# Optimization experiments

Hardware: AMD Instinct MI355X
Metric: run time of the kernel (lower is better)

Reference implementation:

```python
import jax, jax.numpy as jnp
import numpy as np

B, H, S, D = 2, 16, 2048, 64

def setup_inputs() -> dict:
    key = jax.random.key(0)
    kq, kk, kv, km, ks = jax.random.split(key, 5)
    return {
        "query_input": jax.random.normal(kq, (B, H, S, D), dtype=jnp.float32),
        "key_input": jax.random.normal(kk, (B, H, S, D), dtype=jnp.float32),
        "value_input": jax.random.normal(kv, (B, H, S, D), dtype=jnp.float32),
        "query_mask": jnp.ones((B, 1, S, 1), dtype=jnp.float32),
        "key_mask": jax.random.uniform(km, (B, 1, 1, S), dtype=jnp.float32),
        "scale_factor": jax.random.normal(ks, (B, 1, 1, 1), dtype=jnp.float32),
        "dropout": 0,
    }

def reference(query_input, key_input, value_input, query_mask, key_mask, scale_factor, dropout):
    # qk = q @ k^T  -> [B, H, S, S]
    qk = jnp.einsum("bhqd,bhkd->bhqk", query_input, key_input)
    scaled_qk = qk * scale_factor                      # elementwise per-batch scale
    softmax_qk = jax.nn.softmax(scaled_qk, axis=-1)
    masked = softmax_qk * key_mask                     # post-softmax multiplicative mask
    # dropout with p=0 is the identity (deterministic baseline)
    output = jnp.einsum("bhqk,bhkd->bhqd", masked, value_input)
    return output
```

## Files before the change

### kernel.cpp

```cpp
#include <hip/hip_runtime.h>
#include <hip/hip_bf16.h>
#include <stdint.h>

#define BB 2
#define HH 16
#define SS 2048
#define DD 64
constexpr int BH = BB * HH;
constexpr int NT = SS / 64;
constexpr int QB = 16;

typedef _Float16 f16_t;
typedef f16_t f16x8 __attribute__((ext_vector_type(8)));
typedef float f32x4 __attribute__((ext_vector_type(4)));

__device__ __forceinline__ uint32_t pkf16(float a, float b) {
    return __builtin_bit_cast(uint32_t, __builtin_amdgcn_cvt_pkrtz(a, b));
}

__global__ __launch_bounds__(256)
void prepack(const float* __restrict__ Kg, const float* __restrict__ Vg,
             const float* __restrict__ Mg, f16_t* __restrict__ Kp,
             f16_t* __restrict__ Vp)
{
    __shared__ float Vs[64][65];
    const int bh = blockIdx.x % BH;
    const int kt = blockIdx.x / BH;
    const int b  = bh / HH;
    const int t  = threadIdx.x;
    const size_t gbase = (size_t)bh * SS * DD + (size_t)kt * 64 * DD;
    const size_t tbase = ((size_t)bh * NT + kt) * 4096;

    for (int c = t; c < 512; c += 256) {
        const int row = c >> 3, j = c & 7;
        const float* kp = Kg + gbase + (size_t)row * DD + j * 8;
        float4 a = *(const float4*)kp;
        float4 d = *(const float4*)(kp + 4);
        uint4 w = make_uint4(pkf16(a.x, a.y), pkf16(a.z, a.w),
                             pkf16(d.x, d.y), pkf16(d.z, d.w));
        *(uint4*)&Kp[tbase + (size_t)row * 64 + ((j ^ (row & 7)) * 8)] = w;
    }

    for (int c = t; c < 1024; c += 256) {
        const int key = c >> 4, dc = (c & 15) * 4;
        float4 v = *(const float4*)(Vg + gbase + (size_t)key * DD + dc);
        const float m = Mg[(size_t)b * SS + kt * 64 + key];
        Vs[key][dc + 0] = v.x * m;
        Vs[key][dc + 1] = v.y * m;
        Vs[key][dc + 2] = v.z * m;
        Vs[key][dc + 3] = v.w * m;
    }
    __syncthreads();

    for (int c = t; c < 512; c += 256) {
        const int dr = c >> 3, j = c & 7;
        float v0 = Vs[j * 8 + 0][dr], v1 = Vs[j * 8 + 1][dr];
        float v2 = Vs[j * 8 + 2][dr], v3 = Vs[j * 8 + 3][dr];
        float v4 = Vs[j * 8 + 4][dr], v5 = Vs[j * 8 + 5][dr];
        float v6 = Vs[j * 8 + 6][dr], v7 = Vs[j * 8 + 7][dr];
        uint4 w = make_uint4(pkf16(v0, v1), pkf16(v2, v3),
                             pkf16(v4, v5), pkf16(v6, v7));
        *(uint4*)&Vp[tbase + (size_t)dr * 64 + ((j ^ (dr & 7)) * 8)] = w;
    }
}

__global__ __launch_bounds__(512)
void fattn7(const float* __restrict__ Qg, const f16_t* __restrict__ Kp,
            const f16_t* __restrict__ Vp, const float* __restrict__ Sg,
            float* __restrict__ Og)
{
    __shared__ __align__(16) f16_t Kt[2][4096];
    __shared__ __align__(16) f16_t Vt[2][4096];
    __shared__ __align__(16) f16_t Pt[8][16][72];

    const int bh   = blockIdx.x % BH;
    const int qt   = blockIdx.x / BH;
    const int b    = bh / HH;
    const int tid  = threadIdx.x;
    const int wave = tid >> 6;
    const int lane = tid & 63;
    const int l16  = lane & 15;
    const int quad = lane >> 4;

    const float sc = Sg[b] * 1.44269504088896340736f;
    const size_t base = (size_t)bh * SS * DD;
    const size_t tb0  = (size_t)bh * NT * 4096;
    const int q0 = qt * 128 + wave * 16;

    auto stage = [&](int kt, int buf) {
        const f16_t* ks = Kp + tb0 + (size_t)kt * 4096 + tid * 8;
        const f16_t* vs = Vp + tb0 + (size_t)kt * 4096 + tid * 8;
        __builtin_amdgcn_global_load_lds(
            (const __attribute__((address_space(1))) void*)ks,
            (__attribute__((address_space(3))) void*)&Kt[buf][wave * 512],
            16, 0, 0);
        __builtin_amdgcn_global_load_lds(
            (const __attribute__((address_space(1))) void*)vs,
            (__attribute__((address_space(3))) void*)&Vt[buf][wave * 512],
            16, 0, 0);
    };

    stage(0, 0);

    f16x8 qf[2];
    {
        const float* qp = Qg + base + (size_t)(q0 + l16) * DD + quad * 8;
#pragma unroll
        for (int kc = 0; kc < 2; ++kc) {
            float4 a  = *(const float4*)(qp + kc * 32);
            float4 b4 = *(const float4*)(qp + kc * 32 + 4);
            f16x8 f;
            f[0] = (f16_t)(a.x * sc);  f[1] = (f16_t)(a.y * sc);
            f[2] = (f16_t)(a.z * sc);  f[3] = (f16_t)(a.w * sc);
            f[4] = (f16_t)(b4.x * sc); f[5] = (f16_t)(b4.y * sc);
            f[6] = (f16_t)(b4.z * sc); f[7] = (f16_t)(b4.w * sc);
            qf[kc] = f;
        }
    }

    f32x4 Ot[4];
#pragma unroll
    for (int mt = 0; mt < 4; ++mt) Ot[mt] = f32x4{0.f, 0.f, 0.f, 0.f};
    float m_run = -1e30f, l_run = 0.0f;

    const int swz = (l16 & 7) << 3;

    for (int kt = 0; kt < NT; ++kt) {
        const int cur = kt & 1;
        if (kt + 1 < NT) {
            stage(kt + 1, cur ^ 1);
            asm volatile("s_waitcnt vmcnt(2)" ::: "memory");
        } else {
            asm volatile("s_waitcnt vmcnt(0)" ::: "memory");
        }
        __builtin_amdgcn_s_barrier();

        f32x4 Sfr[4];
#pragma unroll
        for (int mt = 0; mt < 4; ++mt) {
            f32x4 acc = f32x4{0.f, 0.f, 0.f, 0.f};
#pragma unroll
            for (int kc = 0; kc < 2; ++kc) {
                const int off = (mt * 16 + l16) * 64 + ((kc * 32 + quad * 8) ^ swz);
                f16x8 kh = *(const f16x8*)&Kt[cur][off];
                acc = __builtin_amdgcn_mfma_f32_16x16x32_f16(kh, qf[kc], acc, 0, 0, 0);
            }
            Sfr[mt] = acc;
        }

        float m0 = fmaxf(fmaxf(Sfr[0][0], Sfr[0][1]), fmaxf(Sfr[0][2], Sfr[0][3]));
        float m1 = fmaxf(fmaxf(Sfr[1][0], Sfr[1][1]), fmaxf(Sfr[1][2], Sfr[1][3]));
        float m2 = fmaxf(fmaxf(Sfr[2][0], Sfr[2][1]), fmaxf(Sfr[2][2], Sfr[2][3]));
        float m3 = fmaxf(fmaxf(Sfr[3][0], Sfr[3][1]), fmaxf(Sfr[3][2], Sfr[3][3]));
        float mx = fmaxf(fmaxf(m0, m1), fmaxf(m2, m3));
        mx = fmaxf(mx, __shfl_xor(mx, 16));
        mx = fmaxf(mx, __shfl_xor(mx, 32));

        if (__any(mx > m_run)) {
            const float mnew  = fmaxf(m_run, mx);
            const float alpha = exp2f(m_run - mnew);
            m_run = mnew;
            l_run *= alpha;
#pragma unroll
            for (int mt = 0; mt < 4; ++mt) Ot[mt] *= alpha;
        }

        float ps[4][4];
        float rs = 0.0f;
#pragma unroll
        for (int mt = 0; mt < 4; ++mt)
#pragma unroll
            for (int r = 0; r < 4; ++r) {
                ps[mt][r] = exp2f(Sfr[mt][r] - m_run);
                rs += ps[mt][r];
            }
        rs += __shfl_xor(rs, 16);
        rs += __shfl_xor(rs, 32);
        l_run += rs;

#pragma unroll
        for (int mt = 0; mt < 4; ++mt) {
            uint2 w = make_uint2(pkf16(ps[mt][0], ps[mt][1]),
                                 pkf16(ps[mt][2], ps[mt][3]));
            *(uint2*)&Pt[wave][l16][mt * 16 + quad * 4] = w;
        }

#pragma unroll
        for (int kc = 0; kc < 2; ++kc) {
            f16x8 pf = *(const f16x8*)&Pt[wave][l16][kc * 32 + quad * 8];
#pragma unroll
            for (int mt = 0; mt < 4; ++mt) {
                const int off = (mt * 16 + l16) * 64 + ((kc * 32 + quad * 8) ^ swz);
                f16x8 vf = *(const f16x8*)&Vt[cur][off];
                Ot[mt] = __builtin_amdgcn_mfma_f32_16x16x32_f16(vf, pf, Ot[mt], 0, 0, 0);
            }
        }
        __builtin_amdgcn_s_barrier();
    }

    const float inv = 1.0f / l_run;
    float* op = Og + base + (size_t)(q0 + l16) * DD + quad * 4;
#pragma unroll
    for (int mt = 0; mt < 4; ++mt) {
#pragma unroll
        for (int r = 0; r < 4; ++r)
            op[mt * 16 + r] = Ot[mt][r] * inv;
    }
}

__global__ __launch_bounds__(512)
void fattn6(const float* __restrict__ Qg, const float* __restrict__ Kg,
            const float* __restrict__ Vg, const float* __restrict__ Mg,
            const float* __restrict__ Sg, float* __restrict__ Og)
{
    __shared__ __align__(16) f16_t Kh_lds[64][72];
    __shared__ __align__(16) f16_t Vt_lds[64][72];
    __shared__ __align__(16) f16_t Pt_lds[8][16][72];
    __shared__ float msk_lds[SS];

    const int bh   = blockIdx.x % BH;
    const int qt   = blockIdx.x / BH;
    const int b    = bh / HH;
    const int tid  = threadIdx.x;
    const int wave = tid >> 6;
    const int lane = tid & 63;
    const int l16  = lane & 15;
    const int quad = lane >> 4;

    const float sc = Sg[b] * 1.44269504088896340736f;
    const size_t base = (size_t)bh * SS * DD;
    const int q0 = qt * 128 + wave * 16;

    for (int i = tid; i < SS; i += 512) msk_lds[i] = Mg[(size_t)b * SS + i];

    f16x8 qf[2];
    {
        const float* qp = Qg + base + (size_t)(q0 + l16) * DD + quad * 8;
#pragma unroll
        for (int kc = 0; kc < 2; ++kc) {
            float4 a  = *(const float4*)(qp + kc * 32);
            float4 b4 = *(const float4*)(qp + kc * 32 + 4);
            f16x8 f;
            f[0] = (f16_t)(a.x * sc);  f[1] = (f16_t)(a.y * sc);
            f[2] = (f16_t)(a.z * sc);  f[3] = (f16_t)(a.w * sc);
            f[4] = (f16_t)(b4.x * sc); f[5] = (f16_t)(b4.y * sc);
            f[6] = (f16_t)(b4.z * sc); f[7] = (f16_t)(b4.w * sc);
            qf[kc] = f;
        }
    }

    f32x4 Ot[4];
#pragma unroll
    for (int mt = 0; mt < 4; ++mt) Ot[mt] = f32x4{0.f, 0.f, 0.f, 0.f};
    float m_run = -1e30f, l_run = 0.0f;

    const int krow = tid >> 3;
    const int kc8  = (tid & 7) * 8;
    const int vd   = tid & 63;
    const int vk0  = (tid >> 6) * 8;

    for (int kt = 0; kt < NT; ++kt) {
        __syncthreads();
        {
            const float* kp = Kg + base + (size_t)(kt * 64 + krow) * DD + kc8;
            float4 a0 = *(const float4*)(kp);
            float4 a1 = *(const float4*)(kp + 4);
            uint4 w = make_uint4(pkf16(a0.x, a0.y), pkf16(a0.z, a0.w),
                                 pkf16(a1.x, a1.y), pkf16(a1.z, a1.w));
            *(uint4*)&Kh_lds[krow][kc8] = w;
        }
        {
            const float* vp = Vg + base + (size_t)(kt * 64 + vk0) * DD + vd;
            const float* mp = &msk_lds[kt * 64 + vk0];
            float v0 = vp[0 * DD] * mp[0], v1 = vp[1 * DD] * mp[1];
            float v2 = vp[2 * DD] * mp[2], v3 = vp[3 * DD] * mp[3];
            float v4 = vp[4 * DD] * mp[4], v5 = vp[5 * DD] * mp[5];
            float v6 = vp[6 * DD] * mp[6], v7 = vp[7 * DD] * mp[7];
            uint4 w = make_uint4(pkf16(v0, v1), pkf16(v2, v3),
                                 pkf16(v4, v5), pkf16(v6, v7));
            *(uint4*)&Vt_lds[vd][vk0] = w;
        }
        __syncthreads();

        f32x4 Sfr[4];
#pragma unroll
        for (int mt = 0; mt < 4; ++mt) {
            f32x4 acc = f32x4{0.f, 0.f, 0.f, 0.f};
#pragma unroll
            for (int kc = 0; kc < 2; ++kc) {
                f16x8 kh = *(const f16x8*)&Kh_lds[mt * 16 + l16][kc * 32 + quad * 8];
                acc = __builtin_amdgcn_mfma_f32_16x16x32_f16(kh, qf[kc], acc, 0, 0, 0);
            }
            Sfr[mt] = acc;
        }

        float mx = Sfr[0][0];
#pragma unroll
        for (int mt = 0; mt < 4; ++mt)
#pragma unroll
            for (int r = 0; r < 4; ++r) mx = fmaxf(mx, Sfr[mt][r]);
        mx = fmaxf(mx, __shfl_xor(mx, 16));
        mx = fmaxf(mx, __shfl_xor(mx, 32));

        if (__any(mx > m_run)) {
            const float mnew  = fmaxf(m_run, mx);
            const float alpha = exp2f(m_run - mnew);
            m_run = mnew;
            l_run *= alpha;
#pragma unroll
            for (int mt = 0; mt < 4; ++mt) Ot[mt] *= alpha;
        }

        float ps[4][4];
        float rs = 0.0f;
#pragma unroll
        for (int mt = 0; mt < 4; ++mt)
#pragma unroll
            for (int r = 0; r < 4; ++r) {
                ps[mt][r] = exp2f(Sfr[mt][r] - m_run);
                rs += ps[mt][r];
            }
        rs += __shfl_xor(rs, 16);
        rs += __shfl_xor(rs, 32);
        l_run += rs;

#pragma unroll
        for (int mt = 0; mt < 4; ++mt) {
            uint2 w = make_uint2(pkf16(ps[mt][0], ps[mt][1]),
                                 pkf16(ps[mt][2], ps[mt][3]));
            *(uint2*)&Pt_lds[wave][l16][mt * 16 + quad * 4] = w;
        }

#pragma unroll
        for (int kc = 0; kc < 2; ++kc) {
            f16x8 pf = *(const f16x8*)&Pt_lds[wave][l16][kc * 32 + quad * 8];
#pragma unroll
            for (int mt = 0; mt < 4; ++mt) {
                f16x8 vf = *(const f16x8*)&Vt_lds[mt * 16 + l16][kc * 32 + quad * 8];
                Ot[mt] = __builtin_amdgcn_mfma_f32_16x16x32_f16(vf, pf, Ot[mt], 0, 0, 0);
            }
        }
    }

    const float inv = 1.0f / l_run;
    float* op = Og + base + (size_t)(q0 + l16) * DD + quad * 4;
#pragma unroll
    for (int mt = 0; mt < 4; ++mt) {
#pragma unroll
        for (int r = 0; r < 4; ++r)
            op[mt * 16 + r] = Ot[mt][r] * inv;
    }
}

extern "C" void kernel_launch(void* const* d_in, const int* in_sizes, int n_in,
                              void* d_out, int out_size, void* d_ws, size_t ws_size,
                              hipStream_t stream) {
    const float* Qg = (const float*)d_in[0];
    const float* Kg = (const float*)d_in[1];
    const float* Vg = (const float*)d_in[2];
    const float* Mg = (const float*)d_in[4];
    const float* Sg = (const float*)d_in[5];
    float* Og = (float*)d_out;

    const size_t kv_elems = (size_t)BH * SS * DD;
    const size_t need = 2 * kv_elems * sizeof(f16_t);

    if (d_ws != nullptr && ws_size >= need) {
        f16_t* Kp = (f16_t*)d_ws;
        f16_t* Vp = Kp + kv_elems;
        prepack<<<dim3(BH * NT), dim3(256), 0, stream>>>(Kg, Vg, Mg, Kp, Vp);
        fattn7<<<dim3(BH * QB), dim3(512), 0, stream>>>(Qg, Kp, Vp, Sg, Og);
    } else {
        fattn6<<<dim3(BH * QB), dim3(512), 0, stream>>>(Qg, Kg, Vg, Mg, Sg, Og);
    }
}
```

Measured before the change: 170.7 us.

## Software-pipeline PV matmul one tile behind QK with triple-buffered V

Restructures the flash-attention loop so the P·V MFMAs for the previous key tile run right after the current tile's QK MFMAs. This lets matrix work overlap the softmax ALU work, with V triple-buffered in LDS and one barrier per iteration instead of two. It also raises wave priority around the MFMA block, skips rescaling unless the running max grows by more than 8 (lazy rescale), and uses the raw hardware exp2 with tree-shaped reductions. The lazy rescale relies on fp16 P values tolerating up to 2^8 growth, and LDS use rises.

```diff
diff --git a/kernel.cpp b/kernel.cpp
--- a/kernel.cpp
+++ b/kernel.cpp
@@ -65,12 +65,12 @@
 }
 
 __global__ __launch_bounds__(512)
-void fattn7(const float* __restrict__ Qg, const f16_t* __restrict__ Kp,
+void fattn8(const float* __restrict__ Qg, const f16_t* __restrict__ Kp,
             const f16_t* __restrict__ Vp, const float* __restrict__ Sg,
             float* __restrict__ Og)
 {
     __shared__ __align__(16) f16_t Kt[2][4096];
-    __shared__ __align__(16) f16_t Vt[2][4096];
+    __shared__ __align__(16) f16_t Vt[3][4096];
     __shared__ __align__(16) f16_t Pt[8][16][72];
 
     const int bh   = blockIdx.x % BH;
@@ -87,20 +87,20 @@
     const size_t tb0  = (size_t)bh * NT * 4096;
     const int q0 = qt * 128 + wave * 16;
 
-    auto stage = [&](int kt, int buf) {
+    auto stage = [&](int kt, int kbuf, int vbuf) {
         const f16_t* ks = Kp + tb0 + (size_t)kt * 4096 + tid * 8;
         const f16_t* vs = Vp + tb0 + (size_t)kt * 4096 + tid * 8;
         __builtin_amdgcn_global_load_lds(
             (const __attribute__((address_space(1))) void*)ks,
-            (__attribute__((address_space(3))) void*)&Kt[buf][wave * 512],
+            (__attribute__((address_space(3))) void*)&Kt[kbuf][wave * 512],
             16, 0, 0);
         __builtin_amdgcn_global_load_lds(
             (const __attribute__((address_space(1))) void*)vs,
-            (__attribute__((address_space(3))) void*)&Vt[buf][wave * 512],
+            (__attribute__((address_space(3))) void*)&Vt[vbuf][wave * 512],
             16, 0, 0);
     };
 
-    stage(0, 0);
+    stage(0, 0, 0);
 
     f16x8 qf[2];
     {
@@ -125,16 +125,19 @@
 
     const int swz = (l16 & 7) << 3;
 
+    int vcur = 0;
     for (int kt = 0; kt < NT; ++kt) {
-        const int cur = kt & 1;
+        const int kcur = kt & 1;
+        const int vnxt = (vcur == 2) ? 0 : vcur + 1;
         if (kt + 1 < NT) {
-            stage(kt + 1, cur ^ 1);
+            stage(kt + 1, kcur ^ 1, vnxt);
             asm volatile("s_waitcnt vmcnt(2)" ::: "memory");
         } else {
             asm volatile("s_waitcnt vmcnt(0)" ::: "memory");
         }
         __builtin_amdgcn_s_barrier();
 
+        __builtin_amdgcn_s_setprio(1);
         f32x4 Sfr[4];
 #pragma unroll
         for (int mt = 0; mt < 4; ++mt) {
@@ -142,23 +145,41 @@
 #pragma unroll
             for (int kc = 0; kc < 2; ++kc) {
                 const int off = (mt * 16 + l16) * 64 + ((kc * 32 + quad * 8) ^ swz);
-                f16x8 kh = *(const f16x8*)&Kt[cur][off];
+                f16x8 kh = *(const f16x8*)&Kt[kcur][off];
                 acc = __builtin_amdgcn_mfma_f32_16x16x32_f16(kh, qf[kc], acc, 0, 0, 0);
             }
             Sfr[mt] = acc;
         }
 
-        float m0 = fmaxf(fmaxf(Sfr[0][0], Sfr[0][1]), fmaxf(Sfr[0][2], Sfr[0][3]));
-        float m1 = fmaxf(fmaxf(Sfr[1][0], Sfr[1][1]), fmaxf(Sfr[1][2], Sfr[1][3]));
-        float m2 = fmaxf(fmaxf(Sfr[2][0], Sfr[2][1]), fmaxf(Sfr[2][2], Sfr[2][3]));
-        float m3 = fmaxf(fmaxf(Sfr[3][0], Sfr[3][1]), fmaxf(Sfr[3][2], Sfr[3][3]));
-        float mx = fmaxf(fmaxf(m0, m1), fmaxf(m2, m3));
+        if (kt > 0) {
+            const int vprv = (vcur == 0) ? 2 : vcur - 1;
+#pragma unroll
+            for (int kc = 0; kc < 2; ++kc) {
+                f16x8 pf = *(const f16x8*)&Pt[wave][l16][kc * 32 + quad * 8];
+#pragma unroll
+                for (int mt = 0; mt < 4; ++mt) {
+                    const int off = (mt * 16 + l16) * 64 + ((kc * 32 + quad * 8) ^ swz);
+                    f16x8 vf = *(const f16x8*)&Vt[vprv][off];
+                    Ot[mt] = __builtin_amdgcn_mfma_f32_16x16x32_f16(vf, pf, Ot[mt], 0, 0, 0);
+                }
+            }
+        }
+        __builtin_amdgcn_s_setprio(0);
+
+        float a0 = fmaxf(fmaxf(Sfr[0][0], Sfr[0][1]), Sfr[0][2]);
+        float b0 = fmaxf(fmaxf(Sfr[1][0], Sfr[1][1]), Sfr[1][2]);
+        a0 = fmaxf(fmaxf(a0, Sfr[0][3]), Sfr[2][0]);
+        b0 = fmaxf(fmaxf(b0, Sfr[1][3]), Sfr[2][1]);
+        a0 = fmaxf(fmaxf(a0, Sfr[2][2]), Sfr[3][0]);
+        b0 = fmaxf(fmaxf(b0, Sfr[2][3]), Sfr[3][1]);
+        a0 = fmaxf(fmaxf(a0, Sfr[3][2]), Sfr[3][3]);
+        float mx = fmaxf(a0, b0);
         mx = fmaxf(mx, __shfl_xor(mx, 16));
         mx = fmaxf(mx, __shfl_xor(mx, 32));
 
-        if (__any(mx > m_run)) {
+        if (__any(mx > m_run + 8.0f)) {
             const float mnew  = fmaxf(m_run, mx);
-            const float alpha = exp2f(m_run - mnew);
+            const float alpha = __builtin_amdgcn_exp2f(m_run - mnew);
             m_run = mnew;
             l_run *= alpha;
 #pragma unroll
@@ -166,14 +187,17 @@
         }
 
         float ps[4][4];
-        float rs = 0.0f;
 #pragma unroll
         for (int mt = 0; mt < 4; ++mt)
 #pragma unroll
-            for (int r = 0; r < 4; ++r) {
-                ps[mt][r] = exp2f(Sfr[mt][r] - m_run);
-                rs += ps[mt][r];
-            }
+            for (int r = 0; r < 4; ++r)
+                ps[mt][r] = __builtin_amdgcn_exp2f(Sfr[mt][r] - m_run);
+
+        float s0 = (ps[0][0] + ps[0][1]) + (ps[0][2] + ps[0][3]);
+        float s1 = (ps[1][0] + ps[1][1]) + (ps[1][2] + ps[1][3]);
+        float s2 = (ps[2][0] + ps[2][1]) + (ps[2][2] + ps[2][3]);
+        float s3 = (ps[3][0] + ps[3][1]) + (ps[3][2] + ps[3][3]);
+        float rs = (s0 + s1) + (s2 + s3);
         rs += __shfl_xor(rs, 16);
         rs += __shfl_xor(rs, 32);
         l_run += rs;
@@ -185,17 +209,22 @@
             *(uint2*)&Pt[wave][l16][mt * 16 + quad * 4] = w;
         }
 
+        __builtin_amdgcn_s_barrier();
+        vcur = vnxt;
+    }
+
+    {
+        const int vprv = (vcur == 0) ? 2 : vcur - 1;
 #pragma unroll
         for (int kc = 0; kc < 2; ++kc) {
             f16x8 pf = *(const f16x8*)&Pt[wave][l16][kc * 32 + quad * 8];
 #pragma unroll
             for (int mt = 0; mt < 4; ++mt) {
                 const int off = (mt * 16 + l16) * 64 + ((kc * 32 + quad * 8) ^ swz);
-                f16x8 vf = *(const f16x8*)&Vt[cur][off];
+                f16x8 vf = *(const f16x8*)&Vt[vprv][off];
                 Ot[mt] = __builtin_amdgcn_mfma_f32_16x16x32_f16(vf, pf, Ot[mt], 0, 0, 0);
             }
         }
-        __builtin_amdgcn_s_barrier();
     }
 
     const float inv = 1.0f / l_run;
@@ -369,7 +398,7 @@
         f16_t* Kp = (f16_t*)d_ws;
         f16_t* Vp = Kp + kv_elems;
         prepack<<<dim3(BH * NT), dim3(256), 0, stream>>>(Kg, Vg, Mg, Kp, Vp);
-        fattn7<<<dim3(BH * QB), dim3(512), 0, stream>>>(Qg, Kp, Vp, Sg, Og);
+        fattn8<<<dim3(BH * QB), dim3(512), 0, stream>>>(Qg, Kp, Vp, Sg, Og);
     } else {
         fattn6<<<dim3(BH * QB), dim3(512), 0, stream>>>(Qg, Kg, Vg, Mg, Sg, Og);
     }
```

Result: faster. 154.7 us (-9.4%).
